# Performance work log

Hardware: AMD Instinct MI355X
Metric: run time of the kernel (lower is better)

Reference implementation:

```python
import jax, jax.numpy as jnp
import numpy as np

N = 512       # nodes
V = 8         # n_vectors_hidden
F = 128       # n_invariant_feat_hidden
H = 8         # num_heads
BESSEL = 8
R_MAX = 10.0
FH = F // H
VH = V // H

def _edges(n):
    s, r = np.meshgrid(np.arange(n), np.arange(n), indexing='ij')
    m = s != r
    return jnp.asarray(s[m], jnp.int32), jnp.asarray(r[m], jnp.int32)

def _sph(v):
    # real spherical harmonics ell=1,2,3, e3nn 'component' normalization, unit input v[...,3] -> [...,15]
    x, y, z = v[..., 0], v[..., 1], v[..., 2]
    s3, s15, s5 = np.sqrt(3.0), np.sqrt(15.0), np.sqrt(5.0)
    sh1 = jnp.stack([x, y, z], -1) * s3
    sh2 = jnp.stack([s15 * x * y, s15 * y * z, 0.5 * s5 * (3 * z**2 - 1), s15 * x * z, 0.5 * s15 * (x**2 - y**2)], -1)
    c33, c32, c31, c30 = np.sqrt(35.0 / 8.0), np.sqrt(105.0), np.sqrt(21.0 / 8.0), 0.5 * np.sqrt(7.0)
    sh3 = jnp.stack([c33 * y * (3 * x**2 - y**2), c32 * x * y * z, c31 * y * (5 * z**2 - 1), c30 * z * (5 * z**2 - 3), c31 * x * (5 * z**2 - 1), 0.5 * c32 * z * (x**2 - y**2), c33 * x * (x**2 - 3 * y**2)], -1)
    return jnp.concatenate([sh1, sh2, sh3], -1)

def _bessel(x, n, x_max):
    # e3nn.bessel basis: sqrt(2/x_max) * sin(k*pi*x/x_max) / x, k=1..n
    x = x[..., None]
    k = jnp.arange(1, n + 1, dtype=x.dtype)
    x_safe = jnp.where(x == 0, 1.0, x)
    return np.sqrt(2.0 / x_max) * jnp.sin(k * jnp.pi * x / x_max) / x_safe

def _sus(x):
    return jnp.where(x > 0, jnp.exp(-1.0 / jnp.where(x > 0, x, 1.0)), 0.0)

def _soft_envelope(x, x_max, a=2.0, v0=1.2):
    return v0 * _sus(a * (1.0 - x / x_max)) / _sus(jnp.asarray(a, x.dtype))

def _forward(positions, features, We0, be0, We1, be1, Wq, Wk, Wek, Wv, Wev, Wg, Wo0, bo0, Wo1, bo1, Wo2, bo2):
    n = positions.shape[0]
    senders, receivers = _edges(n)
    vec = positions[senders] - positions[receivers]               # [E,V,3] gather
    lengths = jnp.sqrt(jnp.sum(vec * vec, -1) + 1e-20)            # safe_norm [E,V]
    unit = vec / lengths[..., None]
    sph = _sph(unit)                                              # [E,V,15]
    radial = _bessel(lengths, BESSEL, R_MAX) * _soft_envelope(lengths, R_MAX)[..., None]  # [E,V,B]
    e_scal = radial.reshape(radial.shape[0], -1)                  # [E, V*B]
    h = jax.nn.silu(e_scal @ We0 + be0)
    h = jax.nn.silu(h @ We1 + be1)                                # edge MLP, output_activation=silu
    E = h.shape[0]
    q = (features @ Wq).reshape(n, H, FH)
    k = (features[senders] @ Wk + h @ Wek).reshape(E, H, FH)
    logits = jnp.einsum('ehf,ehf->eh', q[receivers], k) / np.sqrt(FH)
    seg_max = jax.ops.segment_max(logits, receivers, num_segments=n)
    ex = jnp.exp(logits - seg_max[receivers])                     # edge_weight_cutoff = 1
    denom = jax.ops.segment_sum(ex, receivers, num_segments=n)
    alpha = ex / denom[receivers]                                 # [E,H] per-receiver softmax
    v_s = (features[senders] @ Wv + h @ Wev).reshape(E, H, FH)
    gate = h @ Wg                                                 # [E,V] invariant gates
    v_vec = (gate[..., None] * sph[..., :3]).reshape(E, H, VH, 3) # equivariant values from ell=1 sph
    agg_s = jax.ops.segment_sum(alpha[..., None] * v_s, receivers, num_segments=n).reshape(n, F)
    agg_v = jax.ops.segment_sum(alpha[:, :, None, None] * v_vec, receivers, num_segments=n).reshape(n, V, 3)
    o = jax.nn.silu(agg_s @ Wo0 + bo0)
    o = jax.nn.silu(o @ Wo1 + bo1)
    o = o @ Wo2 + bo2                                             # hk MLP: last layer linear
    return (positions + agg_v, features + o)

def setup_inputs() -> dict:
    key = jax.random.key(0)
    ks = jax.random.split(key, 16)
    def w(k, i, o):
        return jax.random.normal(k, (i, o), jnp.float32) / np.sqrt(i)
    M = 128
    D = V * BESSEL
    return {
        'positions': jax.random.normal(ks[0], (N, V, 3), jnp.float32),
        'features': jax.random.normal(ks[1], (N, F), jnp.float32),
        'We0': w(ks[2], D, M), 'be0': jnp.zeros((M,), jnp.float32),
        'We1': w(ks[3], M, M), 'be1': jnp.zeros((M,), jnp.float32),
        'Wq': w(ks[4], F, F), 'Wk': w(ks[5], F, F), 'Wek': w(ks[6], M, F),
        'Wv': w(ks[7], F, F), 'Wev': w(ks[8], M, F), 'Wg': w(ks[9], M, V),
        'Wo0': w(ks[10], F, M), 'bo0': jnp.zeros((M,), jnp.float32),
        'Wo1': w(ks[11], M, M), 'bo1': jnp.zeros((M,), jnp.float32),
        'Wo2': w(ks[12], M, F), 'bo2': jnp.zeros((F,), jnp.float32),
    }

def reference(positions, features, We0, be0, We1, be1, Wq, Wk, Wek, Wv, Wev, Wg, Wo0, bo0, Wo1, bo1, Wo2, bo2):
    return _forward(positions, features, We0, be0, We1, be1, Wq, Wk, Wek, Wv, Wev, Wg, Wo0, bo0, Wo1, bo1, Wo2, bo2)
```

## Files before the change

### kernel.cpp

```cpp
#include <hip/hip_runtime.h>
#include <hip/hip_bf16.h>

#define WS_KNB  0
#define WS_VNT  32768
#define WS_QNB  65536
#define WS_A4T  98304
#define WS_WGT  360448
#define WS_W0T  360960
#define WS_W1T  365056
#define WS_PS   373248
#define PS_STRIDE 1072

typedef short bf16x8 __attribute__((ext_vector_type(8)));
typedef short short4v __attribute__((ext_vector_type(4)));
typedef float f32x4 __attribute__((ext_vector_type(4)));
typedef unsigned short ushort_t;

static __device__ __forceinline__ ushort_t f2b(float x) {
  __hip_bfloat16 h = __float2bfloat16(x);
  return reinterpret_cast<ushort_t&>(h);
}
static __device__ __forceinline__ float b2f(ushort_t u) {
  unsigned v = ((unsigned)u) << 16;
  return reinterpret_cast<float&>(v);
}
static __device__ __forceinline__ float fsilu(float x) {
  return x * __builtin_amdgcn_rcpf(1.f + __expf(-x));
}

static __device__ __forceinline__ bf16x8 radial_frag(
    float dx, float dy, float dz, float& ux, float& uy, float& uz)
{
  const float l2 = fmaf(dx,dx, fmaf(dy,dy, fmaf(dz,dz, 1e-20f)));
  const float inv = rsqrtf(l2);
  const float len = l2 * inv;
  ux = dx*inv; uy = dy*inv; uz = dz*inv;
  const float yy = 2.f - len*0.2f;
  const float env = (yy > 0.f) ? 1.9784655648f * __expf(-__builtin_amdgcn_rcpf(yy)) : 0.f;
  const float coef = 0.4472135955f * env * inv;
  const float arg = len * 0.31415926535f;
  const float s1v = __sinf(arg), c1v = __cosf(arg);
  const float twc = 2.f*c1v;
  float sp = 0.f, sc = s1v;
  bf16x8 ev;
#pragma unroll
  for (int bb = 0; bb < 8; ++bb) {
    ev[bb] = (short)f2b(coef*sc);
    const float nx = fmaf(twc, sc, -sp);
    sp = sc; sc = nx;
  }
  return ev;
}

__global__ __launch_bounds__(128) void k_prep(
    const float* __restrict__ feat, const float* __restrict__ Wq,
    const float* __restrict__ Wk, const float* __restrict__ Wv,
    const float* __restrict__ Wek, const float* __restrict__ Wg,
    const float* __restrict__ We0, const float* __restrict__ We1,
    float* __restrict__ ws)
{
  const int blk = blockIdx.x, j = threadIdx.x;
  if (blk >= 512) {
    const int i = (blk - 512)*128 + j;
    ushort_t* W0T = (ushort_t*)(ws + WS_W0T);
    ushort_t* W1T = (ushort_t*)(ws + WS_W1T);
    if (i < 8192) {
      const int n = i >> 6, k = i & 63;
      W0T[n*64 + k] = f2b(We0[k*128 + n]);
    } else {
      const int t = i - 8192, n = t >> 7, k = t & 127;
      W1T[n*128 + k] = f2b(We1[k*128 + n]);
    }
    return;
  }
  const int r = blk;
  __shared__ float fr[128];
  __shared__ float qL[128];
  fr[j] = feat[r*128 + j];
  __syncthreads();
  float aq = 0.f, ak = 0.f, av = 0.f;
#pragma unroll 4
  for (int i = 0; i < 128; ++i) {
    const float f = fr[i];
    aq = fmaf(f, Wq[i*128 + j], aq);
    ak = fmaf(f, Wk[i*128 + j], ak);
    av = fmaf(f, Wv[i*128 + j], av);
  }
  ushort_t* knB = (ushort_t*)(ws + WS_KNB);
  ushort_t* vnT = (ushort_t*)(ws + WS_VNT);
  ushort_t* qnB = (ushort_t*)(ws + WS_QNB);
  knB[r*128 + j] = f2b(ak);
  vnT[j*512 + r] = f2b(av);
  qnB[r*128 + j] = f2b(0.25f * aq);
  qL[j] = aq;
  __syncthreads();
  ushort_t* A4 = (ushort_t*)(ws + WS_A4T) + r*1024;
  const float* wr = Wek + j*128;
#pragma unroll
  for (int h = 0; h < 8; ++h) {
    float acc = 0.f;
#pragma unroll
    for (int f = 0; f < 16; ++f)
      acc = fmaf(wr[16*h + f], qL[16*h + f], acc);
    A4[h*128 + j] = f2b(acc * 0.25f);
  }
  if (r == 0) {
    ushort_t* WgT = (ushort_t*)(ws + WS_WGT);
#pragma unroll
    for (int v = 0; v < 8; ++v)
      WgT[v*128 + j] = f2b(Wg[j*8 + v]);
  }
}

#define MFMA(a,b,c) __builtin_amdgcn_mfma_f32_16x16x32_bf16((a),(b),(c),0,0,0)

__global__ __launch_bounds__(512, 4) void k_edge17(
    const float* __restrict__ pos,
    const float* __restrict__ be0, const float* __restrict__ be1,
    float* __restrict__ ws)
{
  __shared__ __align__(16) char Lds[40960];
  ushort_t* H1   = (ushort_t*)(Lds);
  ushort_t* Pb   = (ushort_t*)(Lds);
  float*    rscL = (float*)(Lds + 2048);
  ushort_t* H2t  = (ushort_t*)(Lds + 16384);
  ushort_t* Es   = (ushort_t*)(Lds + 32768);
  float*    lgT0 = (float*)(Lds + 32768);
  float*    lgT1 = (float*)(Lds + 36864);

  const int tid = threadIdx.x;
  const int nw = tid >> 6, l = tid & 63;
  const int c = l & 15, g = l >> 4;
  const int b = blockIdx.x;
  const int r = b >> 2, quarter = b & 3;
  const int base = quarter * 128;

  const ushort_t* knB = (const ushort_t*)(ws + WS_KNB);
  const ushort_t* vnT = (const ushort_t*)(ws + WS_VNT);
  const ushort_t* qnB = (const ushort_t*)(ws + WS_QNB);
  const ushort_t* A4G = (const ushort_t*)(ws + WS_A4T) + r*1024;
  const ushort_t* WgG = (const ushort_t*)(ws + WS_WGT);
  const ushort_t* W0T = (const ushort_t*)(ws + WS_W0T);
  const ushort_t* W1T = (const ushort_t*)(ws + WS_W1T);

  const int ncol = nw*16 + c;
  const float be0v = be0[ncol], be1v = be1[ncol];
  const int m_lg = nw & 3, kh = nw >> 2;
  const int ncswz = ((ncol & 7) ^ ((ncol >> 3) & 7)) & 7;

  const float prx = pos[r*24 + nw*3 + 0];
  const float pry = pos[r*24 + nw*3 + 1];
  const float prz = pos[r*24 + nw*3 + 2];

  f32x4 bh = {0,0,0,0}, sna = {0,0,0,0};
  float avx = 0.f, avy = 0.f, avz = 0.f;
  float mrun = -1e30f, drun = 0.f;
  float ux, uy, uz;

  {
    const int sg = base + l;
    const bf16x8 ev = radial_frag(pos[sg*24 + nw*3 + 0] - prx,
                                  pos[sg*24 + nw*3 + 1] - pry,
                                  pos[sg*24 + nw*3 + 2] - prz, ux, uy, uz);
    *(bf16x8*)(Es + l*64 + ((nw ^ (l&7))<<3)) = ev;
  }
  __syncthreads();

  for (int tile = 0; tile < 2; ++tile) {
    const int gbase = base + tile*64;

    float npx = 0.f, npy = 0.f, npz = 0.f;
    if (tile < 1) {
      const int sg = gbase + 64 + l;
      npx = pos[sg*24 + nw*3 + 0];
      npy = pos[sg*24 + nw*3 + 1];
      npz = pos[sg*24 + nw*3 + 2];
    }

    {
      const bf16x8 w0f0 = *(const bf16x8*)(W0T + ncol*64 + g*8);
      const bf16x8 w0f1 = *(const bf16x8*)(W0T + ncol*64 + 32 + g*8);
#pragma unroll
      for (int m = 0; m < 4; ++m) {
        const int ra = m*16 + c;
        const bf16x8 e0 = *(const bf16x8*)(Es + ra*64 + (((g  ) ^ (ra&7))<<3));
        const bf16x8 e1 = *(const bf16x8*)(Es + ra*64 + (((4+g) ^ (ra&7))<<3));
        f32x4 acc = {0,0,0,0};
        acc = MFMA(e0, w0f0, acc);
        acc = MFMA(e1, w0f1, acc);
#pragma unroll
        for (int i = 0; i < 4; ++i) {
          const int row = m*16 + g*4 + i;
          H1[row*128 + (((ncol>>3) ^ (row&15))<<3) + (c&7)] =
              f2b(fsilu(acc[i] + be0v));
        }
      }
    }
    __syncthreads();

#pragma unroll
    for (int m = 0; m < 4; ++m) {
      const int ra = m*16 + c;
      f32x4 acc = {0,0,0,0};
#pragma unroll
      for (int kb = 0; kb < 4; ++kb) {
        const bf16x8 af = *(const bf16x8*)(H1 + ra*128 + (((kb*4+g) ^ (ra&15))<<3));
        const bf16x8 wf = *(const bf16x8*)(W1T + ncol*128 + kb*32 + g*8);
        acc = MFMA(af, wf, acc);
      }
      short4v pk;
#pragma unroll
      for (int i = 0; i < 4; ++i)
        pk[i] = (short)f2b(fsilu(acc[i] + be1v));
      *(short4v*)(H2t + ncol*64 +
          ((((m*2 + (g>>1)) ^ ncswz) & 7)<<3) + (g&1)*4) = pk;
    }
    __syncthreads();

    {
      f32x4 lg = {0,0,0,0};
      if (kh == 0) {
        const int rb = m_lg*2 + (c>>3);
        const int rl = c & 7;
        const ushort_t* ab = (c < 8) ? (A4G + c*128) : (WgG + (c-8)*128);
#pragma unroll
        for (int kb = 0; kb < 4; ++kb) {
          const int cc = (kb*4 + g) & 7;
          bf16x8 bb;
#pragma unroll
          for (int j = 0; j < 8; ++j)
            bb[j] = (short)H2t[(kb*32 + g*8 + j)*64 +
                               (((rb ^ j ^ cc) & 7)<<3) + rl];
          const bf16x8 aw = *(const bf16x8*)(ab + kb*32 + g*8);
          lg = MFMA(aw, bb, lg);
        }
      } else {
        const int srow = gbase + m_lg*16 + c;
#pragma unroll
        for (int kb = 0; kb < 4; ++kb) {
          const bf16x8 bb = *(const bf16x8*)(knB + srow*128 + kb*32 + g*8);
          const bf16x8 qf = *(const bf16x8*)(qnB + r*128 + kb*32 + g*8);
          bf16x8 aw;
          const bool hit = (kb*2 + (g>>1)) == c;
#pragma unroll
          for (int j = 0; j < 8; ++j) aw[j] = hit ? qf[j] : (short)0;
          lg = MFMA(aw, bb, lg);
        }
      }
      float* lgW = kh ? lgT1 : lgT0;
#pragma unroll
      for (int i = 0; i < 4; ++i) {
        const int ch = g*4 + i;
        lgW[ch*64 + ((m_lg*16 + c) ^ (g<<4))] = lg[i];
      }
    }
    __syncthreads();

    {
      const int h = nw;
      const int kv = (h>>2)<<4;
      const int kg = ((8+h)>>2)<<4;
      float lgv = lgT0[h*64 + (l ^ kv)] + lgT1[h*64 + (l ^ kv)];
      const float gate = lgT0[(8+h)*64 + (l ^ kg)] + lgT1[(8+h)*64 + (l ^ kg)];
      if (gbase + l == r) lgv = -1e30f;
      float t = lgv;
      t = fmaxf(t, __shfl_xor(t, 1));
      t = fmaxf(t, __shfl_xor(t, 2));
      t = fmaxf(t, __shfl_xor(t, 4));
      t = fmaxf(t, __shfl_xor(t, 8));
      t = fmaxf(t, __shfl_xor(t, 16));
      t = fmaxf(t, __shfl_xor(t, 32));
      const float mnew = fmaxf(mrun, t);
      const float rsc = __expf(mrun - mnew);
      mrun = mnew;
      const float val = __expf(lgv - mnew);
      float wsm = val;
      wsm += __shfl_xor(wsm, 1);
      wsm += __shfl_xor(wsm, 2);
      wsm += __shfl_xor(wsm, 4);
      wsm += __shfl_xor(wsm, 8);
      wsm += __shfl_xor(wsm, 16);
      wsm += __shfl_xor(wsm, 32);
      drun = drun*rsc + wsm;
      const float ga = val * gate;
      Pb[h*64 + (((l>>3) ^ h)<<3) + (l&7)] = f2b(val);
      Pb[(8+h)*64 + (((l>>3) ^ h)<<3) + (l&7)] = f2b(ga);
      if (l == 0) rscL[h] = rsc;
      avx = avx*rsc + ga*ux;
      avy = avy*rsc + ga*uy;
      avz = avz*rsc + ga*uz;
    }
    __syncthreads();

    {
      float rs[4];
#pragma unroll
      for (int i = 0; i < 4; ++i) rs[i] = rscL[(4*g + i) & 7];
#pragma unroll
      for (int i = 0; i < 4; ++i) { bh[i] *= rs[i]; sna[i] *= rs[i]; }
      const bf16x8 pa0 = *(const bf16x8*)(Pb + c*64 + (((g  ) ^ (c&7))<<3));
      const bf16x8 pa1 = *(const bf16x8*)(Pb + c*64 + (((4+g) ^ (c&7))<<3));
      bh = MFMA(pa0, *(const bf16x8*)(H2t + ncol*64 +
               ((((g  ) ^ ncswz) & 7)<<3)), bh);
      bh = MFMA(pa1, *(const bf16x8*)(H2t + ncol*64 +
               ((((4+g) ^ ncswz) & 7)<<3)), bh);
      const bf16x8 vnf0 = *(const bf16x8*)(vnT + ncol*512 + gbase + g*8);
      const bf16x8 vnf1 = *(const bf16x8*)(vnT + ncol*512 + gbase + 32 + g*8);
      sna = MFMA(pa0, vnf0, sna);
      sna = MFMA(pa1, vnf1, sna);
    }
    if (tile < 1) {
      const bf16x8 ev = radial_frag(npx - prx, npy - pry, npz - prz, ux, uy, uz);
      *(bf16x8*)(Es + l*64 + ((nw ^ (l&7))<<3)) = ev;
      __syncthreads();
    }
  }

  float* PSf = ws + WS_PS + b*PS_STRIDE;
  ushort_t* PSs = (ushort_t*)PSf;
  if (g < 2) {
#pragma unroll
    for (int i = 0; i < 4; ++i) {
      PSs[(4*g + i)*128 + ncol] = f2b(bh[i]);
      PSs[1024 + (4*g + i)*128 + ncol] = f2b(sna[i]);
    }
  }
  avx += __shfl_xor(avx, 1); avy += __shfl_xor(avy, 1); avz += __shfl_xor(avz, 1);
  avx += __shfl_xor(avx, 2); avy += __shfl_xor(avy, 2); avz += __shfl_xor(avz, 2);
  avx += __shfl_xor(avx, 4); avy += __shfl_xor(avy, 4); avz += __shfl_xor(avz, 4);
  avx += __shfl_xor(avx, 8); avy += __shfl_xor(avy, 8); avz += __shfl_xor(avz, 8);
  avx += __shfl_xor(avx,16); avy += __shfl_xor(avy,16); avz += __shfl_xor(avz,16);
  avx += __shfl_xor(avx,32); avy += __shfl_xor(avy,32); avz += __shfl_xor(avz,32);
  if (l == 0) {
    PSf[1024 + nw*3 + 0] = avx;
    PSf[1024 + nw*3 + 1] = avy;
    PSf[1024 + nw*3 + 2] = avz;
    PSf[1048 + nw] = mrun;
    PSf[1056 + nw] = drun;
  }
}

__global__ __launch_bounds__(128) void k_merge(
    const float* __restrict__ pos, const float* __restrict__ feat,
    const float* __restrict__ Wev,
    const float* __restrict__ Wo0, const float* __restrict__ bo0,
    const float* __restrict__ Wo1, const float* __restrict__ bo1,
    const float* __restrict__ Wo2, const float* __restrict__ bo2,
    const float* __restrict__ ws, float* __restrict__ out)
{
  const int r = blockIdx.x, j = threadIdx.x;
  __shared__ float Ss[32], Dh[8];
  __shared__ float BhC[1024];
  __shared__ float asB[128], o1[128], o2[128];
  const float* Pf[4];
  const ushort_t* Ps[4];
#pragma unroll
  for (int i = 0; i < 4; ++i) {
    Pf[i] = ws + WS_PS + (4*r + i)*PS_STRIDE;
    Ps[i] = (const ushort_t*)Pf[i];
  }
  if (j < 8) {
    float M = -1e30f;
#pragma unroll
    for (int i = 0; i < 4; ++i) M = fmaxf(M, Pf[i][1048 + j]);
    float D = 0.f;
#pragma unroll
    for (int i = 0; i < 4; ++i) {
      const float s = __expf(Pf[i][1048 + j] - M);
      Ss[i*8 + j] = s;
      D = fmaf(s, Pf[i][1056 + j], D);
    }
    Dh[j] = D;
  }
  __syncthreads();
#pragma unroll
  for (int h = 0; h < 8; ++h) {
    float acc = 0.f;
#pragma unroll
    for (int i = 0; i < 4; ++i)
      acc = fmaf(Ss[i*8 + h], b2f(Ps[i][h*128 + j]), acc);
    BhC[h*128 + j] = acc;
  }
  const int hh = j >> 4;
  float snj = 0.f;
#pragma unroll
  for (int i = 0; i < 4; ++i)
    snj = fmaf(Ss[i*8 + hh], b2f(Ps[i][1024 + hh*128 + j]), snj);
  if (j < 24) {
    const int v = j / 3;
    float avc = 0.f;
#pragma unroll
    for (int i = 0; i < 4; ++i)
      avc = fmaf(Ss[i*8 + v], Pf[i][1024 + j], avc);
    out[r*24 + j] = pos[r*24 + j]
        + 1.7320508076f * avc * __builtin_amdgcn_rcpf(Dh[v]);
  }
  __syncthreads();
  {
    float ev = 0.f;
#pragma unroll 4
    for (int m = 0; m < 128; ++m)
      ev = fmaf(BhC[hh*128 + m], Wev[m*128 + j], ev);
    asB[j] = (snj + ev) * __builtin_amdgcn_rcpf(Dh[hh]);
  }
  __syncthreads();
  {
    float acc = bo0[j];
#pragma unroll 4
    for (int i = 0; i < 128; ++i) acc = fmaf(asB[i], Wo0[i*128 + j], acc);
    o1[j] = fsilu(acc);
  }
  __syncthreads();
  {
    float acc = bo1[j];
#pragma unroll 4
    for (int i = 0; i < 128; ++i) acc = fmaf(o1[i], Wo1[i*128 + j], acc);
    o2[j] = fsilu(acc);
  }
  __syncthreads();
  {
    float acc = bo2[j];
#pragma unroll 4
    for (int i = 0; i < 128; ++i) acc = fmaf(o2[i], Wo2[i*128 + j], acc);
    out[12288 + r*128 + j] = feat[r*128 + j] + acc;
  }
}

extern "C" void kernel_launch(void* const* d_in, const int* in_sizes, int n_in,
                              void* d_out, int out_size, void* d_ws, size_t ws_size,
                              hipStream_t stream)
{
  const float* pos  = (const float*)d_in[0];
  const float* feat = (const float*)d_in[1];
  const float* We0  = (const float*)d_in[2];
  const float* be0  = (const float*)d_in[3];
  const float* We1  = (const float*)d_in[4];
  const float* be1  = (const float*)d_in[5];
  const float* Wq   = (const float*)d_in[6];
  const float* Wk   = (const float*)d_in[7];
  const float* Wek  = (const float*)d_in[8];
  const float* Wv   = (const float*)d_in[9];
  const float* Wev  = (const float*)d_in[10];
  const float* Wg   = (const float*)d_in[11];
  const float* Wo0  = (const float*)d_in[12];
  const float* bo0  = (const float*)d_in[13];
  const float* Wo1  = (const float*)d_in[14];
  const float* bo1  = (const float*)d_in[15];
  const float* Wo2  = (const float*)d_in[16];
  const float* bo2  = (const float*)d_in[17];
  float* ws  = (float*)d_ws;
  float* out = (float*)d_out;

  hipLaunchKernelGGL(k_prep, dim3(704), dim3(128), 0, stream,
                     feat, Wq, Wk, Wv, Wek, Wg, We0, We1, ws);
  hipLaunchKernelGGL(k_edge17, dim3(2048), dim3(512), 0, stream,
                     pos, be0, be1, ws);
  hipLaunchKernelGGL(k_merge, dim3(512), dim3(128), 0, stream,
                     pos, feat, Wev, Wo0, bo0, Wo1, bo1, Wo2, bo2, ws, out);
}
```

Baseline: 101.5 us.

## Software-pipeline edge kernel over 32-edge tiles with double-buffered LDS stages

Restructures the edge kernel from two 64-edge tiles with four barriers each into four 32-edge tiles in a staged pipeline. Radial basis, layer-0, layer-1, logits/softmax and PV stages of different tiles are interleaved between two barriers per step, with double-buffered Es/H2t in LDS. Logit weight fragments are hoisted into registers before the loop, and unit vectors are recomputed inside the softmax stage. Only half of each wave's lanes does the radial and softmax work, and only half the waves compute logits, so some lane utilization is lost in exchange for fewer barriers. The occupancy hint in launch bounds is also dropped.

```diff
diff --git a/kernel.cpp b/kernel.cpp
--- a/kernel.cpp
+++ b/kernel.cpp
@@ -28,13 +28,12 @@
   return x * __builtin_amdgcn_rcpf(1.f + __expf(-x));
 }
 
-static __device__ __forceinline__ bf16x8 radial_frag(
-    float dx, float dy, float dz, float& ux, float& uy, float& uz)
+static __device__ __forceinline__ bf16x8 radial_only(
+    float dx, float dy, float dz)
 {
   const float l2 = fmaf(dx,dx, fmaf(dy,dy, fmaf(dz,dz, 1e-20f)));
   const float inv = rsqrtf(l2);
   const float len = l2 * inv;
-  ux = dx*inv; uy = dy*inv; uz = dz*inv;
   const float yy = 2.f - len*0.2f;
   const float env = (yy > 0.f) ? 1.9784655648f * __expf(-__builtin_amdgcn_rcpf(yy)) : 0.f;
   const float coef = 0.4472135955f * env * inv;
@@ -114,19 +113,19 @@
 
 #define MFMA(a,b,c) __builtin_amdgcn_mfma_f32_16x16x32_bf16((a),(b),(c),0,0,0)
 
-__global__ __launch_bounds__(512, 4) void k_edge17(
+__global__ __launch_bounds__(512) void k_edge18(
     const float* __restrict__ pos,
     const float* __restrict__ be0, const float* __restrict__ be1,
     float* __restrict__ ws)
 {
-  __shared__ __align__(16) char Lds[40960];
-  ushort_t* H1   = (ushort_t*)(Lds);
-  ushort_t* Pb   = (ushort_t*)(Lds);
-  float*    rscL = (float*)(Lds + 2048);
+  __shared__ __align__(16) char Lds[37920];
+  ushort_t* Es   = (ushort_t*)(Lds);
+  ushort_t* H1   = (ushort_t*)(Lds + 8192);
   ushort_t* H2t  = (ushort_t*)(Lds + 16384);
-  ushort_t* Es   = (ushort_t*)(Lds + 32768);
   float*    lgT0 = (float*)(Lds + 32768);
-  float*    lgT1 = (float*)(Lds + 36864);
+  float*    lgT1 = (float*)(Lds + 34816);
+  ushort_t* Pb   = (ushort_t*)(Lds + 36864);
+  float*    rscL = (float*)(Lds + 37888);
 
   const int tid = threadIdx.x;
   const int nw = tid >> 6, l = tid & 63;
@@ -145,8 +144,28 @@
 
   const int ncol = nw*16 + c;
   const float be0v = be0[ncol], be1v = be1[ncol];
-  const int m_lg = nw & 3, kh = nw >> 2;
-  const int ncswz = ((ncol & 7) ^ ((ncol >> 3) & 7)) & 7;
+  const int m_lg = nw & 1, kh = (nw >> 1) & 1;
+  const int csw = ((ncol & 3) ^ ((ncol >> 2) & 3)) & 3;
+
+  const bf16x8 w0f0 = *(const bf16x8*)(W0T + ncol*64 + g*8);
+  const bf16x8 w0f1 = *(const bf16x8*)(W0T + ncol*64 + 32 + g*8);
+  bf16x8 awf[4];
+  if (nw < 4) {
+    if (kh == 0) {
+      const ushort_t* ab = (c < 8) ? (A4G + c*128) : (WgG + (c-8)*128);
+#pragma unroll
+      for (int kb = 0; kb < 4; ++kb)
+        awf[kb] = *(const bf16x8*)(ab + kb*32 + g*8);
+    } else {
+#pragma unroll
+      for (int kb = 0; kb < 4; ++kb) {
+        const bf16x8 qf = *(const bf16x8*)(qnB + r*128 + kb*32 + g*8);
+        const bool hit = (kb*2 + (g>>1)) == c;
+#pragma unroll
+        for (int j = 0; j < 8; ++j) awf[kb][j] = hit ? qf[j] : (short)0;
+      }
+    }
+  }
 
   const float prx = pos[r*24 + nw*3 + 0];
   const float pry = pos[r*24 + nw*3 + 1];
@@ -155,51 +174,38 @@
   f32x4 bh = {0,0,0,0}, sna = {0,0,0,0};
   float avx = 0.f, avy = 0.f, avz = 0.f;
   float mrun = -1e30f, drun = 0.f;
-  float ux, uy, uz;
-
-  {
-    const int sg = base + l;
-    const bf16x8 ev = radial_frag(pos[sg*24 + nw*3 + 0] - prx,
-                                  pos[sg*24 + nw*3 + 1] - pry,
-                                  pos[sg*24 + nw*3 + 2] - prz, ux, uy, uz);
-    *(bf16x8*)(Es + l*64 + ((nw ^ (l&7))<<3)) = ev;
-  }
-  __syncthreads();
-
-  for (int tile = 0; tile < 2; ++tile) {
-    const int gbase = base + tile*64;
-
-    float npx = 0.f, npy = 0.f, npz = 0.f;
-    if (tile < 1) {
-      const int sg = gbase + 64 + l;
-      npx = pos[sg*24 + nw*3 + 0];
-      npy = pos[sg*24 + nw*3 + 1];
-      npz = pos[sg*24 + nw*3 + 2];
-    }
-
-    {
-      const bf16x8 w0f0 = *(const bf16x8*)(W0T + ncol*64 + g*8);
-      const bf16x8 w0f1 = *(const bf16x8*)(W0T + ncol*64 + 32 + g*8);
-#pragma unroll
-      for (int m = 0; m < 4; ++m) {
-        const int ra = m*16 + c;
-        const bf16x8 e0 = *(const bf16x8*)(Es + ra*64 + (((g  ) ^ (ra&7))<<3));
-        const bf16x8 e1 = *(const bf16x8*)(Es + ra*64 + (((4+g) ^ (ra&7))<<3));
-        f32x4 acc = {0,0,0,0};
-        acc = MFMA(e0, w0f0, acc);
-        acc = MFMA(e1, w0f1, acc);
-#pragma unroll
-        for (int i = 0; i < 4; ++i) {
-          const int row = m*16 + g*4 + i;
-          H1[row*128 + (((ncol>>3) ^ (row&15))<<3) + (c&7)] =
-              f2b(fsilu(acc[i] + be0v));
-        }
+
+  auto G = [&](int k) {
+    if (l < 32) {
+      const int s = base + k*32 + l;
+      const bf16x8 ev = radial_only(pos[s*24 + nw*3 + 0] - prx,
+                                    pos[s*24 + nw*3 + 1] - pry,
+                                    pos[s*24 + nw*3 + 2] - prz);
+      *(bf16x8*)(Es + (k&1)*2048 + l*64 + ((nw ^ (l&7))<<3)) = ev;
+    }
+  };
+  auto L0 = [&](int k) {
+    const ushort_t* E = Es + (k&1)*2048;
+#pragma unroll
+    for (int m = 0; m < 2; ++m) {
+      const int ra = m*16 + c;
+      const bf16x8 e0 = *(const bf16x8*)(E + ra*64 + (((g  ) ^ (ra&7))<<3));
+      const bf16x8 e1 = *(const bf16x8*)(E + ra*64 + (((4+g) ^ (ra&7))<<3));
+      f32x4 acc = {0,0,0,0};
+      acc = MFMA(e0, w0f0, acc);
+      acc = MFMA(e1, w0f1, acc);
+#pragma unroll
+      for (int i = 0; i < 4; ++i) {
+        const int row = m*16 + g*4 + i;
+        H1[row*128 + (((ncol>>3) ^ (row&15))<<3) + (c&7)] =
+            f2b(fsilu(acc[i] + be0v));
       }
     }
-    __syncthreads();
-
-#pragma unroll
-    for (int m = 0; m < 4; ++m) {
+  };
+  auto L1 = [&](int k) {
+    ushort_t* HT = H2t + (k&1)*4096;
+#pragma unroll
+    for (int m = 0; m < 2; ++m) {
       const int ra = m*16 + c;
       f32x4 acc = {0,0,0,0};
 #pragma unroll
@@ -212,64 +218,53 @@
 #pragma unroll
       for (int i = 0; i < 4; ++i)
         pk[i] = (short)f2b(fsilu(acc[i] + be1v));
-      *(short4v*)(H2t + ncol*64 +
-          ((((m*2 + (g>>1)) ^ ncswz) & 7)<<3) + (g&1)*4) = pk;
-    }
-    __syncthreads();
-
-    {
-      f32x4 lg = {0,0,0,0};
-      if (kh == 0) {
-        const int rb = m_lg*2 + (c>>3);
-        const int rl = c & 7;
-        const ushort_t* ab = (c < 8) ? (A4G + c*128) : (WgG + (c-8)*128);
-#pragma unroll
-        for (int kb = 0; kb < 4; ++kb) {
-          const int cc = (kb*4 + g) & 7;
-          bf16x8 bb;
-#pragma unroll
-          for (int j = 0; j < 8; ++j)
-            bb[j] = (short)H2t[(kb*32 + g*8 + j)*64 +
-                               (((rb ^ j ^ cc) & 7)<<3) + rl];
-          const bf16x8 aw = *(const bf16x8*)(ab + kb*32 + g*8);
-          lg = MFMA(aw, bb, lg);
+      const int chnk = m*2 + (g>>1);
+      *(short4v*)(HT + ncol*32 + (((chnk ^ csw) & 3)<<3) + (g&1)*4) = pk;
+    }
+  };
+  auto LG = [&](int k) {
+    if (nw >= 4) return;
+    const ushort_t* HT = H2t + (k&1)*4096;
+    f32x4 lg = {0,0,0,0};
+    if (kh == 0) {
+      const int sb = m_lg*2 + (c>>3);
+      const int si = c & 7;
+#pragma unroll
+      for (int kb = 0; kb < 4; ++kb) {
+        bf16x8 bb;
+#pragma unroll
+        for (int j = 0; j < 8; ++j) {
+          const int f = kb*32 + g*8 + j;
+          bb[j] = (short)HT[f*32 + (((sb ^ (f&3) ^ ((f>>2)&3)) & 3)<<3) + si];
         }
-      } else {
-        const int srow = gbase + m_lg*16 + c;
-#pragma unroll
-        for (int kb = 0; kb < 4; ++kb) {
-          const bf16x8 bb = *(const bf16x8*)(knB + srow*128 + kb*32 + g*8);
-          const bf16x8 qf = *(const bf16x8*)(qnB + r*128 + kb*32 + g*8);
-          bf16x8 aw;
-          const bool hit = (kb*2 + (g>>1)) == c;
-#pragma unroll
-          for (int j = 0; j < 8; ++j) aw[j] = hit ? qf[j] : (short)0;
-          lg = MFMA(aw, bb, lg);
-        }
+        lg = MFMA(awf[kb], bb, lg);
       }
-      float* lgW = kh ? lgT1 : lgT0;
-#pragma unroll
-      for (int i = 0; i < 4; ++i) {
-        const int ch = g*4 + i;
-        lgW[ch*64 + ((m_lg*16 + c) ^ (g<<4))] = lg[i];
+    } else {
+      const int srow = base + k*32 + m_lg*16 + c;
+#pragma unroll
+      for (int kb = 0; kb < 4; ++kb) {
+        const bf16x8 bb = *(const bf16x8*)(knB + srow*128 + kb*32 + g*8);
+        lg = MFMA(awf[kb], bb, lg);
       }
     }
-    __syncthreads();
-
-    {
+    float* lgW = kh ? lgT1 : lgT0;
+#pragma unroll
+    for (int i = 0; i < 4; ++i)
+      lgW[(g*4 + i)*32 + m_lg*16 + c] = lg[i];
+  };
+  auto SM = [&](int k) {
+    if (l < 32) {
       const int h = nw;
-      const int kv = (h>>2)<<4;
-      const int kg = ((8+h)>>2)<<4;
-      float lgv = lgT0[h*64 + (l ^ kv)] + lgT1[h*64 + (l ^ kv)];
-      const float gate = lgT0[(8+h)*64 + (l ^ kg)] + lgT1[(8+h)*64 + (l ^ kg)];
-      if (gbase + l == r) lgv = -1e30f;
+      const int s = base + k*32 + l;
+      float lgv = lgT0[h*32 + l] + lgT1[h*32 + l];
+      const float gate = lgT0[(8+h)*32 + l] + lgT1[(8+h)*32 + l];
+      if (s == r) lgv = -1e30f;
       float t = lgv;
       t = fmaxf(t, __shfl_xor(t, 1));
       t = fmaxf(t, __shfl_xor(t, 2));
       t = fmaxf(t, __shfl_xor(t, 4));
       t = fmaxf(t, __shfl_xor(t, 8));
       t = fmaxf(t, __shfl_xor(t, 16));
-      t = fmaxf(t, __shfl_xor(t, 32));
       const float mnew = fmaxf(mrun, t);
       const float rsc = __expf(mrun - mnew);
       mrun = mnew;
@@ -280,41 +275,50 @@
       wsm += __shfl_xor(wsm, 4);
       wsm += __shfl_xor(wsm, 8);
       wsm += __shfl_xor(wsm, 16);
-      wsm += __shfl_xor(wsm, 32);
       drun = drun*rsc + wsm;
       const float ga = val * gate;
-      Pb[h*64 + (((l>>3) ^ h)<<3) + (l&7)] = f2b(val);
-      Pb[(8+h)*64 + (((l>>3) ^ h)<<3) + (l&7)] = f2b(ga);
+      Pb[h*32 + ((((l>>3) ^ (h&3)) & 3)<<3) + (l&7)] = f2b(val);
+      Pb[(8+h)*32 + ((((l>>3) ^ (h&3)) & 3)<<3) + (l&7)] = f2b(ga);
       if (l == 0) rscL[h] = rsc;
-      avx = avx*rsc + ga*ux;
-      avy = avy*rsc + ga*uy;
-      avz = avz*rsc + ga*uz;
-    }
+      const float dx = pos[s*24 + h*3 + 0] - prx;
+      const float dy = pos[s*24 + h*3 + 1] - pry;
+      const float dz = pos[s*24 + h*3 + 2] - prz;
+      const float inv = rsqrtf(fmaf(dx,dx, fmaf(dy,dy, fmaf(dz,dz, 1e-20f))));
+      avx = avx*rsc + ga*dx*inv;
+      avy = avy*rsc + ga*dy*inv;
+      avz = avz*rsc + ga*dz*inv;
+    }
+  };
+  auto PV = [&](int k) {
+    const ushort_t* HT = H2t + (k&1)*4096;
+    float rs[4];
+#pragma unroll
+    for (int i = 0; i < 4; ++i) rs[i] = rscL[(4*g + i) & 7];
+#pragma unroll
+    for (int i = 0; i < 4; ++i) { bh[i] *= rs[i]; sna[i] *= rs[i]; }
+    const bf16x8 pa = *(const bf16x8*)(Pb + c*32 + (((g ^ (c&3)) & 3)<<3));
+    bh  = MFMA(pa, *(const bf16x8*)(HT + ncol*32 + (((g ^ csw) & 3)<<3)), bh);
+    sna = MFMA(pa, *(const bf16x8*)(vnT + ncol*512 + base + k*32 + g*8), sna);
+  };
+
+  G(0);
+  __syncthreads();
+  L0(0); G(1);
+  __syncthreads();
+  L1(0);
+  __syncthreads();
+#pragma unroll
+  for (int k = 0; k < 4; ++k) {
+    if (k >= 1) PV(k-1);
+    LG(k);
+    if (k+1 < 4) L0(k+1);
+    if (k+2 < 4) G(k+2);
     __syncthreads();
-
-    {
-      float rs[4];
-#pragma unroll
-      for (int i = 0; i < 4; ++i) rs[i] = rscL[(4*g + i) & 7];
-#pragma unroll
-      for (int i = 0; i < 4; ++i) { bh[i] *= rs[i]; sna[i] *= rs[i]; }
-      const bf16x8 pa0 = *(const bf16x8*)(Pb + c*64 + (((g  ) ^ (c&7))<<3));
-      const bf16x8 pa1 = *(const bf16x8*)(Pb + c*64 + (((4+g) ^ (c&7))<<3));
-      bh = MFMA(pa0, *(const bf16x8*)(H2t + ncol*64 +
-               ((((g  ) ^ ncswz) & 7)<<3)), bh);
-      bh = MFMA(pa1, *(const bf16x8*)(H2t + ncol*64 +
-               ((((4+g) ^ ncswz) & 7)<<3)), bh);
-      const bf16x8 vnf0 = *(const bf16x8*)(vnT + ncol*512 + gbase + g*8);
-      const bf16x8 vnf1 = *(const bf16x8*)(vnT + ncol*512 + gbase + 32 + g*8);
-      sna = MFMA(pa0, vnf0, sna);
-      sna = MFMA(pa1, vnf1, sna);
-    }
-    if (tile < 1) {
-      const bf16x8 ev = radial_frag(npx - prx, npy - pry, npz - prz, ux, uy, uz);
-      *(bf16x8*)(Es + l*64 + ((nw ^ (l&7))<<3)) = ev;
-      __syncthreads();
-    }
-  }
+    SM(k);
+    if (k+1 < 4) L1(k+1);
+    __syncthreads();
+  }
+  PV(3);
 
   float* PSf = ws + WS_PS + b*PS_STRIDE;
   ushort_t* PSs = (ushort_t*)PSf;
@@ -330,7 +334,6 @@
   avx += __shfl_xor(avx, 4); avy += __shfl_xor(avy, 4); avz += __shfl_xor(avz, 4);
   avx += __shfl_xor(avx, 8); avy += __shfl_xor(avy, 8); avz += __shfl_xor(avz, 8);
   avx += __shfl_xor(avx,16); avy += __shfl_xor(avy,16); avz += __shfl_xor(avz,16);
-  avx += __shfl_xor(avx,32); avy += __shfl_xor(avy,32); avz += __shfl_xor(avz,32);
   if (l == 0) {
     PSf[1024 + nw*3 + 0] = avx;
     PSf[1024 + nw*3 + 1] = avy;
@@ -453,7 +456,7 @@
 
   hipLaunchKernelGGL(k_prep, dim3(704), dim3(128), 0, stream,
                      feat, Wq, Wk, Wv, Wek, Wg, We0, We1, ws);
-  hipLaunchKernelGGL(k_edge17, dim3(2048), dim3(512), 0, stream,
+  hipLaunchKernelGGL(k_edge18, dim3(2048), dim3(512), 0, stream,
                      pos, be0, be1, ws);
   hipLaunchKernelGGL(k_merge, dim3(512), dim3(128), 0, stream,
                      pos, feat, Wev, Wo0, bo0, Wo1, bo1, Wo2, bo2, ws, out);
```

Result: slower. 144.5 us (+42.4%).
